# Optimization experiments

Hardware: AMD Instinct MI355X
Metric: run time of the kernel (lower is better)

## Reference

```python
import jax, jax.numpy as jnp
import numpy as np

PATCH = 768
POS = 64
HID = 512
B, N = 8, 2048


def setup_inputs() -> dict:
    key = jax.random.key(0)
    ks = jax.random.split(key, 8)
    d_in = PATCH + POS
    s = 1.0 / np.sqrt(d_in)
    return {
        "patches": jax.random.normal(ks[0], (B, N, PATCH), jnp.float32),
        "positions": jax.random.normal(ks[1], (B, N, POS), jnp.float32),
        "Wq": jax.random.uniform(ks[2], (d_in, HID), jnp.float32, -s, s),
        "bq": jax.random.uniform(ks[3], (HID,), jnp.float32, -s, s),
        "Wk": jax.random.uniform(ks[4], (d_in, HID), jnp.float32, -s, s),
        "bk": jax.random.uniform(ks[5], (d_in and HID,), jnp.float32, -s, s),
        "Wv": jax.random.uniform(ks[6], (d_in, HID), jnp.float32, -s, s),
        "bv": jax.random.uniform(ks[7], (HID,), jnp.float32, -s, s),
    }


def reference(patches, positions, Wq, bq, Wk, bk, Wv, bv):
    # concat patch features with positional features: [B, N, PATCH+POS]
    x = jnp.concatenate([patches, positions], axis=-1)
    Q = x @ Wq + bq  # [B, N, HID]
    K = x @ Wk + bk
    V = x @ Wv + bv
    scale = jnp.sqrt(jnp.asarray(HID, x.dtype))
    scores = jnp.einsum("bnd,bmd->bnm", Q, K) / scale  # [B, N, N]
    weights = jax.nn.softmax(scores, axis=-1)
    return jnp.einsum("bnm,bmd->bnd", weights, V)  # [B, N, HID]
```

## Files before the change

kernel.cpp:

```cpp
#include <hip/hip_runtime.h>
#include <hip/hip_bf16.h>
#include <math.h>

typedef __hip_bfloat16 bf16;
typedef __attribute__((ext_vector_type(4))) float f32x4;
typedef __attribute__((ext_vector_type(8))) short s16x8;

typedef const __attribute__((address_space(1))) void gvoid_t;
typedef __attribute__((address_space(3))) void lvoid_t;

__device__ __forceinline__ void gload16(const void* g, void* l) {
  __builtin_amdgcn_global_load_lds((gvoid_t*)g, (lvoid_t*)l, 16, 0, 0);
}
__device__ __forceinline__ unsigned short f2b(float f) {
  bf16 h = __float2bfloat16(f);
  return *(unsigned short*)&h;
}

__global__ __launch_bounds__(256) void prep_x(const float* __restrict__ patches,
                                              const float* __restrict__ positions,
                                              bf16* __restrict__ xb) {
  const int c = threadIdx.x;
  const bool lo = (c < 192);
  const bool hi = (c >= 192) && (c < 208);
  if (!(lo || hi)) return;
  const int dst = lo ? (c * 4) : (768 + (c - 192) * 4);
  #pragma unroll
  for (int rr = 0; rr < 8; ++rr) {
    const long long row = (long long)blockIdx.x * 8 + rr;
    const float* src = lo ? (patches + row * 768 + c * 4)
                          : (positions + row * 64 + (c - 192) * 4);
    float4 v = *(const float4*)src;
    uint2 w;
    w.x = (unsigned int)f2b(v.x) | ((unsigned int)f2b(v.y) << 16);
    w.y = (unsigned int)f2b(v.z) | ((unsigned int)f2b(v.w) << 16);
    *(uint2*)(xb + row * 832 + dst) = w;
  }
}

__global__ __launch_bounds__(256) void prep_w(const float* __restrict__ Wq,
                                              const float* __restrict__ Wk,
                                              const float* __restrict__ Wv,
                                              bf16* __restrict__ Wt) {
  __shared__ float tile[32][33];
  const int z = blockIdx.z;
  const float* W = (z == 0) ? Wq : (z == 1) ? Wk : Wv;
  bf16* T = Wt + (long long)z * 512 * 832;
  const int n0 = blockIdx.x * 32;
  const int k0 = blockIdx.y * 32;
  const int tx = threadIdx.x, ty = threadIdx.y;
  #pragma unroll
  for (int i = 0; i < 32; i += 8)
    tile[ty + i][tx] = W[(long long)(k0 + ty + i) * 512 + n0 + tx];
  __syncthreads();
  #pragma unroll
  for (int i = 0; i < 32; i += 8)
    T[(long long)(n0 + ty + i) * 832 + k0 + tx] = __float2bfloat16(tile[tx][ty + i]);
}

#define VMW5  asm volatile("s_waitcnt vmcnt(5)" ::: "memory")
#define VMW8  asm volatile("s_waitcnt vmcnt(8)" ::: "memory")
#define VMW10 asm volatile("s_waitcnt vmcnt(10)" ::: "memory")
#define PBAR do { __builtin_amdgcn_s_barrier(); __builtin_amdgcn_sched_barrier(0); } while (0)

__device__ __forceinline__ void stage_half(const bf16* src, char* lds, int stride) {
  gload16(src, lds);
  gload16(src + 64 * stride, lds + 8192);
}
__device__ __forceinline__ void stage_b192(const bf16* src, char* lds) {
  gload16(src, lds);
  gload16(src + 64 * 832, lds + 8192);
  gload16(src + 128 * 832, lds + 16384);
}
__device__ __forceinline__ void lda4(const bf16* base, int rowbase, int llo,
                                     int xk0, int xk1, s16x8 af[4][2]) {
  #pragma unroll
  for (int mf = 0; mf < 4; mf++) {
    const bf16* p = base + (rowbase + mf * 16 + llo) * 64;
    af[mf][0] = *(const s16x8*)(p + xk0);
    af[mf][1] = *(const s16x8*)(p + xk1);
  }
}
__device__ __forceinline__ void ldb2(const bf16* base, int rowbase, int llo,
                                     int xk0, int xk1, s16x8 bfr[2][2]) {
  #pragma unroll
  for (int nf = 0; nf < 2; nf++) {
    const bf16* p = base + (rowbase + nf * 16 + llo) * 64;
    bfr[nf][0] = *(const s16x8*)(p + xk0);
    bfr[nf][1] = *(const s16x8*)(p + xk1);
  }
}
__device__ __forceinline__ void ldb3(const bf16* base, int rowbase, int llo,
                                     int xk0, int xk1, s16x8 bfr[3][2]) {
  #pragma unroll
  for (int nf = 0; nf < 3; nf++) {
    const bf16* p = base + (rowbase + nf * 16 + llo) * 64;
    bfr[nf][0] = *(const s16x8*)(p + xk0);
    bfr[nf][1] = *(const s16x8*)(p + xk1);
  }
}
__device__ __forceinline__ void mma16(f32x4 acc[4][2], s16x8 af[4][2],
                                      s16x8 bfr[2][2]) {
  __builtin_amdgcn_s_setprio(1);
  #pragma unroll
  for (int mf = 0; mf < 4; mf++)
    #pragma unroll
    for (int nf = 0; nf < 2; nf++) {
      acc[mf][nf] = __builtin_amdgcn_mfma_f32_16x16x32_bf16(
          af[mf][0], bfr[nf][0], acc[mf][nf], 0, 0, 0);
      acc[mf][nf] = __builtin_amdgcn_mfma_f32_16x16x32_bf16(
          af[mf][1], bfr[nf][1], acc[mf][nf], 0, 0, 0);
    }
  __builtin_amdgcn_s_setprio(0);
}
__device__ __forceinline__ void mma24(f32x4 acc[4][3], s16x8 af[4][2],
                                      s16x8 bfr[3][2]) {
  __builtin_amdgcn_s_setprio(1);
  #pragma unroll
  for (int mf = 0; mf < 4; mf++)
    #pragma unroll
    for (int nf = 0; nf < 3; nf++) {
      acc[mf][nf] = __builtin_amdgcn_mfma_f32_16x16x32_bf16(
          af[mf][0], bfr[nf][0], acc[mf][nf], 0, 0, 0);
      acc[mf][nf] = __builtin_amdgcn_mfma_f32_16x16x32_bf16(
          af[mf][1], bfr[nf][1], acc[mf][nf], 0, 0, 0);
    }
  __builtin_amdgcn_s_setprio(0);
}

#define QKV_TILE(abuf, bbuf, bstage, ka1, kb2)                               \
  do {                                                                       \
                                                               \
    lda4(As2[abuf], wm * 64, llo, xk0, xk1, af);                             \
    ldb3(Bs3[bbuf], wn * 48, llo, xk0, xk1, bfr);                            \
    stage_half(sA + (ka1), (char*)As2[(abuf) ^ 1] + wofs, 832);              \
    stage_b192(sB + (kb2), (char*)Bs3[bstage] + wofs);                       \
    VMW5; PBAR;                                                              \
    mma24(acc[0], af, bfr);                                                  \
                               \
    lda4(As2[abuf], 128 + wm * 64, llo, xk0, xk1, af);                       \
    stage_half(sA + 128 * 832 + (ka1), (char*)As2[(abuf) ^ 1] + 16384 + wofs,\
               832);                                                         \
    VMW5; PBAR;                                                              \
    mma24(acc[1], af, bfr);                                                  \
  } while (0)

__global__ __launch_bounds__(512, 2) void gemm_qkv(
    const bf16* __restrict__ xb, const bf16* __restrict__ Wt,
    const float* __restrict__ bq, const float* __restrict__ bk,
    const float* __restrict__ bv,
    bf16* __restrict__ qk, bf16* __restrict__ vt) {
  __shared__ bf16 As2[2][256 * 64];
  __shared__ bf16 Bs3[3][192 * 64];
  const int tid = threadIdx.x;
  const int wave = tid >> 6, lane = tid & 63;
  const int llo = lane & 15, lhi = lane >> 4;
  const int wm = wave >> 2, wn = wave & 3;

  const unsigned int lin = blockIdx.x;
  const unsigned int xcd = lin & 7u, idx = lin >> 3;
  const unsigned int g = xcd * 64u + idx;
  const int bm_t = (int)(g >> 3);
  const int bn_t = (int)(g & 7u);
  const int row0 = bm_t * 256;
  const int col0 = bn_t * 192;

  const int sr = tid >> 3;
  const int kkofs = ((tid & 7) ^ (sr & 7)) << 3;
  const bf16* sA = xb + (long long)(row0 + sr) * 832 + kkofs;
  const bf16* sB = Wt + (long long)(col0 + sr) * 832 + kkofs;
  const int wofs = wave * 1024;

  const int xk0 = ((lhi ^ (llo & 7)) << 3);
  const int xk1 = (((4 + lhi) ^ (llo & 7)) << 3);

  f32x4 acc[2][4][3] = {};
  s16x8 af[4][2], bfr[3][2];

  stage_half(sA, (char*)As2[0] + wofs, 832);
  stage_b192(sB, (char*)Bs3[0] + wofs);
  stage_half(sA + 128 * 832, (char*)As2[0] + 16384 + wofs, 832);
  stage_b192(sB + 64, (char*)Bs3[1] + wofs);
  VMW5; PBAR;

  for (int jj = 0; jj < 2; ++jj) {
    const int u0 = jj * 6;
    QKV_TILE(0, 0, 2, (u0 + 1) * 64, (u0 + 2) * 64);
    QKV_TILE(1, 1, 0, (u0 + 2) * 64, (u0 + 3) * 64);
    QKV_TILE(0, 2, 1, (u0 + 3) * 64, (u0 + 4) * 64);
    QKV_TILE(1, 0, 2, (u0 + 4) * 64, (u0 + 5) * 64);
    QKV_TILE(0, 1, 0, (u0 + 5) * 64, (u0 + 6) * 64);
    QKV_TILE(1, 2, 1, (u0 + 6) * 64, ((u0 + 7) <= 12 ? (u0 + 7) * 64 : 768));
  }
  QKV_TILE(0, 0, 2, 768, 768);

  asm volatile("s_waitcnt vmcnt(0)" ::: "memory");

  #pragma unroll
  for (int qr = 0; qr < 2; qr++)
    #pragma unroll
    for (int mf = 0; mf < 4; mf++)
      #pragma unroll
      for (int nf = 0; nf < 3; nf++) {
        const int c = col0 + wn * 48 + nf * 16 + llo;
        const int z = c >> 9, cc = c & 511;
        const int grow0 = row0 + qr * 128 + wm * 64 + mf * 16 + lhi * 4;
        if (z < 2) {
          const float bb = (z ? bk : bq)[cc];
          bf16* outp = qk + (long long)z * 16384 * 512;
          #pragma unroll
          for (int r = 0; r < 4; r++)
            outp[(long long)(grow0 + r) * 512 + cc] =
                __float2bfloat16(acc[qr][mf][nf][r] + bb);
        } else {
          const int b = grow0 >> 11, j = grow0 & 2047;
          const float bb = bv[cc];
          uint2 w;
          w.x = (unsigned int)f2b(acc[qr][mf][nf][0] + bb) |
                ((unsigned int)f2b(acc[qr][mf][nf][1] + bb) << 16);
          w.y = (unsigned int)f2b(acc[qr][mf][nf][2] + bb) |
                ((unsigned int)f2b(acc[qr][mf][nf][3] + bb) << 16);
          *(uint2*)(vt + (long long)b * 512 * 2048 + (long long)cc * 2048 + j) = w;
        }
      }
}
#undef QKV_TILE

__global__ __launch_bounds__(512, 2) void gemm_scores(const bf16* __restrict__ qk,
                                                      bf16* __restrict__ S,
                                                      float* __restrict__ rowsumP) {
  __shared__ bf16 As[2][256 * 64];
  __shared__ bf16 Bs[2][256 * 64];
  const int tid = threadIdx.x;
  const int wave = tid >> 6, lane = tid & 63;
  const int llo = lane & 15, lhi = lane >> 4;
  const int wm = wave >> 2, wn = wave & 3;

  const unsigned int lin = blockIdx.x;
  const int b = (int)(lin & 7u);
  const unsigned int idx = lin >> 3;
  const int row0 = (int)(idx >> 3) * 256;
  const int coltile = (int)(idx & 7u);
  const int col0 = coltile * 256;

  const bf16* Ab = qk + (long long)b * 2048 * 512;
  const bf16* Bb = qk + (long long)16384 * 512 + (long long)b * 2048 * 512;

  const int sr = tid >> 3;
  const int kkofs = ((tid & 7) ^ (sr & 7)) << 3;
  const bf16* sA = Ab + (long long)(row0 + sr) * 512 + kkofs;
  const bf16* sB = Bb + (long long)(col0 + sr) * 512 + kkofs;
  const int wofs = wave * 1024;

  const int xk0 = ((lhi ^ (llo & 7)) << 3);
  const int xk1 = (((4 + lhi) ^ (llo & 7)) << 3);

  f32x4 acc[2][2][4][2] = {};
  s16x8 af[4][2], bf0[2][2], bf1[2][2];

  stage_half(sA, (char*)As[0] + wofs, 512);
  stage_half(sB, (char*)Bs[0] + wofs, 512);
  stage_half(sB + 128 * 512, (char*)Bs[0] + 16384 + wofs, 512);
  stage_half(sA + 128 * 512, (char*)As[0] + 16384 + wofs, 512);
  stage_half(sA + 64, (char*)As[1] + wofs, 512);
  stage_half(sB + 64, (char*)Bs[1] + wofs, 512);
  VMW8; PBAR;

  for (int i = 0; i < 4; ++i) {
    const int kt1 = (2 * i + 1) * 64;
    const int kt2 = (2 * i + 2 < 8) ? (2 * i + 2) * 64 : 448;
    const int kt3 = (2 * i + 3 < 8) ? (2 * i + 3) * 64 : 448;
    lda4(As[0], wm * 64, llo, xk0, xk1, af);
    ldb2(Bs[0], wn * 32, llo, xk0, xk1, bf0);
    stage_half(sB + 128 * 512 + kt1, (char*)Bs[1] + 16384 + wofs, 512);
    VMW8; PBAR;
    mma16(acc[0][0], af, bf0);
    ldb2(Bs[0], 128 + wn * 32, llo, xk0, xk1, bf1);
    stage_half(sA + 128 * 512 + kt1, (char*)As[1] + 16384 + wofs, 512);
    VMW8; PBAR;
    mma16(acc[0][1], af, bf1);
    lda4(As[0], 128 + wm * 64, llo, xk0, xk1, af);
    stage_half(sA + kt2, (char*)As[0] + wofs, 512);
    PBAR;
    mma16(acc[1][0], af, bf0);
    stage_half(sB + kt2, (char*)Bs[0] + wofs, 512);
    VMW8; PBAR;
    mma16(acc[1][1], af, bf1);
    lda4(As[1], wm * 64, llo, xk0, xk1, af);
    ldb2(Bs[1], wn * 32, llo, xk0, xk1, bf0);
    stage_half(sB + 128 * 512 + kt2, (char*)Bs[0] + 16384 + wofs, 512);
    VMW8; PBAR;
    mma16(acc[0][0], af, bf0);
    ldb2(Bs[1], 128 + wn * 32, llo, xk0, xk1, bf1);
    stage_half(sA + 128 * 512 + kt2, (char*)As[0] + 16384 + wofs, 512);
    VMW8; PBAR;
    mma16(acc[0][1], af, bf1);
    lda4(As[1], 128 + wm * 64, llo, xk0, xk1, af);
    stage_half(sA + kt3, (char*)As[1] + wofs, 512);
    PBAR;
    mma16(acc[1][0], af, bf0);
    stage_half(sB + kt3, (char*)Bs[1] + wofs, 512);
    VMW8; PBAR;
    mma16(acc[1][1], af, bf1);
  }

  __syncthreads();

  const float alpha = 0.044194173824159216f;
  bf16* Sb = S + (long long)b * 2048 * 2048;
  #pragma unroll
  for (int qr = 0; qr < 2; qr++)
    #pragma unroll
    for (int qc = 0; qc < 2; qc++)
      #pragma unroll
      for (int mf = 0; mf < 4; mf++)
        #pragma unroll
        for (int nf = 0; nf < 2; nf++) {
          #pragma unroll
          for (int r = 0; r < 4; r++)
            acc[qr][qc][mf][nf][r] = __expf(acc[qr][qc][mf][nf][r] * alpha);
          const int gcol = col0 + qc * 128 + wn * 32 + nf * 16 + llo;
          const int grow0 = row0 + qr * 128 + wm * 64 + mf * 16 + lhi * 4;
          #pragma unroll
          for (int r = 0; r < 4; r++)
            Sb[(long long)(grow0 + r) * 2048 + gcol] =
                __float2bfloat16(acc[qr][qc][mf][nf][r]);
        }

  float* psum = (float*)As;
  #pragma unroll
  for (int qr = 0; qr < 2; qr++)
    #pragma unroll
    for (int mf = 0; mf < 4; mf++)
      #pragma unroll
      for (int r = 0; r < 4; r++) {
        float p = acc[qr][0][mf][0][r] + acc[qr][0][mf][1][r] +
                  acc[qr][1][mf][0][r] + acc[qr][1][mf][1][r];
        p += __shfl_xor(p, 1, 64);
        p += __shfl_xor(p, 2, 64);
        p += __shfl_xor(p, 4, 64);
        p += __shfl_xor(p, 8, 64);
        if (llo == 0)
          psum[wn * 256 + qr * 128 + wm * 64 + mf * 16 + lhi * 4 + r] = p;
      }
  __syncthreads();
  if (tid < 256) {
    const float v = psum[tid] + psum[256 + tid] + psum[512 + tid] + psum[768 + tid];
    rowsumP[(long long)(b * 8 + coltile) * 2048 + row0 + tid] = v;
  }
}

__global__ __launch_bounds__(256) void reduce_rowsum(
    const float* __restrict__ rowsumP, float* __restrict__ rinv) {
  const int i = blockIdx.x * 256 + threadIdx.x;
  const int b = i >> 11, row = i & 2047;
  const float* p = rowsumP + ((long long)b * 8) * 2048 + row;
  float s = 0.f;
  #pragma unroll
  for (int t = 0; t < 8; t++) s += p[t * 2048];
  rinv[i] = 1.0f / s;
}

#define PV_TILE(c, cs, kstage)                                              \
  do {                                                                      \
                                                              \
    lda4(As3[c], wm * 64, llo, xk0, xk1, af);                               \
    ldb2(Bs3[c], wn * 32, llo, xk0, xk1, bfr);                              \
    stage_half(sA + (kstage), (char*)As3[cs] + wofs, 2048);                 \
    stage_half(sB + (kstage), (char*)Bs3[cs] + wofs, 2048);                 \
    VMW10; PBAR;                                                            \
    mma16(acc[0], af, bfr);                                                 \
                              \
    lda4(As3[c], 128 + wm * 64, llo, xk0, xk1, af);                         \
    stage_half(sA + 128 * 2048 + (kstage), (char*)As3[cs] + 16384 + wofs,   \
               2048);                                                       \
    VMW8; PBAR;                                                             \
    mma16(acc[1], af, bfr);                                                 \
  } while (0)

__global__ __launch_bounds__(512, 2) void gemm_pv(const bf16* __restrict__ S,
                                                  const bf16* __restrict__ vt,
                                                  const float* __restrict__ rinv,
                                                  float* __restrict__ out) {
  __shared__ bf16 As3[3][256 * 64];
  __shared__ bf16 Bs3[3][128 * 64];
  const int tid = threadIdx.x;
  const int wave = tid >> 6, lane = tid & 63;
  const int llo = lane & 15, lhi = lane >> 4;
  const int wm = wave >> 2, wn = wave & 3;

  const unsigned int lin = blockIdx.x;
  const int b = (int)(lin & 7u);
  const unsigned int idx = lin >> 3;
  const int row0 = (int)(idx >> 2) * 256;
  const int col0 = (int)(idx & 3u) * 128;

  const bf16* Ab = S + (long long)b * 2048 * 2048;
  const bf16* Bb = vt + (long long)b * 512 * 2048;

  const int sr = tid >> 3;
  const int kkofs = ((tid & 7) ^ (sr & 7)) << 3;
  const bf16* sA = Ab + (long long)(row0 + sr) * 2048 + kkofs;
  const bf16* sB = Bb + (long long)(col0 + sr) * 2048 + kkofs;
  const int wofs = wave * 1024;

  const int xk0 = ((lhi ^ (llo & 7)) << 3);
  const int xk1 = (((4 + lhi) ^ (llo & 7)) << 3);

  f32x4 acc[2][4][2] = {};
  s16x8 af[4][2], bfr[2][2];

  stage_half(sA, (char*)As3[0] + wofs, 2048);
  stage_half(sB, (char*)Bs3[0] + wofs, 2048);
  stage_half(sA + 128 * 2048, (char*)As3[0] + 16384 + wofs, 2048);
  stage_half(sA + 64, (char*)As3[1] + wofs, 2048);
  stage_half(sB + 64, (char*)Bs3[1] + wofs, 2048);
  stage_half(sA + 128 * 2048 + 64, (char*)As3[1] + 16384 + wofs, 2048);
  VMW8; PBAR;

  for (int j = 0; j < 10; ++j) {
    const int kb = j * 192;
    PV_TILE(0, 2, kb + 128);
    PV_TILE(1, 0, kb + 192);
    PV_TILE(2, 1, kb + 256);
  }
  PV_TILE(0, 2, 1984);
  PV_TILE(1, 0, 1984);

  asm volatile("s_waitcnt vmcnt(0)" ::: "memory");

  const float* rs = rinv + (long long)b * 2048;
  float* Ob = out + (long long)b * 2048 * 512;
  #pragma unroll
  for (int qr = 0; qr < 2; qr++)
    #pragma unroll
    for (int mf = 0; mf < 4; mf++) {
      const int grow0 = row0 + qr * 128 + wm * 64 + mf * 16 + lhi * 4;
      float iv[4];
      #pragma unroll
      for (int r = 0; r < 4; r++) iv[r] = rs[grow0 + r];
      #pragma unroll
      for (int nf = 0; nf < 2; nf++) {
        const int gcol = col0 + wn * 32 + nf * 16 + llo;
        #pragma unroll
        for (int r = 0; r < 4; r++)
          Ob[(long long)(grow0 + r) * 512 + gcol] = acc[qr][mf][nf][r] * iv[r];
      }
    }
}
#undef PV_TILE

extern "C" void kernel_launch(void* const* d_in, const int* in_sizes, int n_in,
                              void* d_out, int out_size, void* d_ws, size_t ws_size,
                              hipStream_t stream) {
  const float* patches = (const float*)d_in[0];
  const float* positions = (const float*)d_in[1];
  const float* Wq = (const float*)d_in[2];
  const float* bq = (const float*)d_in[3];
  const float* Wk = (const float*)d_in[4];
  const float* bk = (const float*)d_in[5];
  const float* Wv = (const float*)d_in[6];
  const float* bv = (const float*)d_in[7];
  float* out = (float*)d_out;

  if (ws_size < 149422080u) return;

  char* ws = (char*)d_ws;
  bf16* Wt = (bf16*)(ws);
  bf16* xb = (bf16*)(ws + 2555904);
  bf16* qk = (bf16*)(ws + 29818880);
  bf16* vt = (bf16*)(ws + 63373312);
  bf16* S  = (bf16*)(ws + 80150528);
  float* rinv    = (float*)(ws + 147259392);
  float* rowsumP = (float*)(ws + 147324928);

  prep_x<<<2048, 256, 0, stream>>>(patches, positions, xb);
  prep_w<<<dim3(16, 26, 3), dim3(32, 8), 0, stream>>>(Wq, Wk, Wv, Wt);
  gemm_qkv<<<512, 512, 0, stream>>>(xb, Wt, bq, bk, bv, qk, vt);
  gemm_scores<<<512, 512, 0, stream>>>(qk, S, rowsumP);
  reduce_rowsum<<<64, 256, 0, stream>>>(rowsumP, rinv);
  gemm_pv<<<256, 512, 0, stream>>>(S, vt, rinv, out);
}
```

Measured before the change: 262.1 us.

## Retile QKV GEMM to 256x128 with triple buffering and fuse rowsum reduction into PV

The QKV projection GEMM moves from 256x192 tiles with A double-buffered to 256x128 tiles with both A and B triple-buffered, and launches 768 blocks instead of 512. Each tile now maps to a single Q/K/V matrix, so the epilogue branch is taken once per block instead of per fragment. The separate reduce_rowsum kernel is removed; gemm_pv sums the partial row sums itself after its main loop and stores the reciprocals in LDS, saving one launch at the cost of a little redundant work per block. Smaller tiles reuse A less per block, traded for more blocks and a deeper pipeline.

```diff
diff --git a/kernel.cpp b/kernel.cpp
--- a/kernel.cpp
+++ b/kernel.cpp
@@ -58,7 +58,6 @@
     T[(long long)(n0 + ty + i) * 832 + k0 + tx] = __float2bfloat16(tile[tx][ty + i]);
 }
 
-#define VMW5  asm volatile("s_waitcnt vmcnt(5)" ::: "memory")
 #define VMW8  asm volatile("s_waitcnt vmcnt(8)" ::: "memory")
 #define VMW10 asm volatile("s_waitcnt vmcnt(10)" ::: "memory")
 #define PBAR do { __builtin_amdgcn_s_barrier(); __builtin_amdgcn_sched_barrier(0); } while (0)
@@ -66,11 +65,6 @@
 __device__ __forceinline__ void stage_half(const bf16* src, char* lds, int stride) {
   gload16(src, lds);
   gload16(src + 64 * stride, lds + 8192);
-}
-__device__ __forceinline__ void stage_b192(const bf16* src, char* lds) {
-  gload16(src, lds);
-  gload16(src + 64 * 832, lds + 8192);
-  gload16(src + 128 * 832, lds + 16384);
 }
 __device__ __forceinline__ void lda4(const bf16* base, int rowbase, int llo,
                                      int xk0, int xk1, s16x8 af[4][2]) {
@@ -85,15 +79,6 @@
                                      int xk0, int xk1, s16x8 bfr[2][2]) {
   #pragma unroll
   for (int nf = 0; nf < 2; nf++) {
-    const bf16* p = base + (rowbase + nf * 16 + llo) * 64;
-    bfr[nf][0] = *(const s16x8*)(p + xk0);
-    bfr[nf][1] = *(const s16x8*)(p + xk1);
-  }
-}
-__device__ __forceinline__ void ldb3(const bf16* base, int rowbase, int llo,
-                                     int xk0, int xk1, s16x8 bfr[3][2]) {
-  #pragma unroll
-  for (int nf = 0; nf < 3; nf++) {
     const bf16* p = base + (rowbase + nf * 16 + llo) * 64;
     bfr[nf][0] = *(const s16x8*)(p + xk0);
     bfr[nf][1] = *(const s16x8*)(p + xk1);
@@ -113,36 +98,22 @@
     }
   __builtin_amdgcn_s_setprio(0);
 }
-__device__ __forceinline__ void mma24(f32x4 acc[4][3], s16x8 af[4][2],
-                                      s16x8 bfr[3][2]) {
-  __builtin_amdgcn_s_setprio(1);
-  #pragma unroll
-  for (int mf = 0; mf < 4; mf++)
-    #pragma unroll
-    for (int nf = 0; nf < 3; nf++) {
-      acc[mf][nf] = __builtin_amdgcn_mfma_f32_16x16x32_bf16(
-          af[mf][0], bfr[nf][0], acc[mf][nf], 0, 0, 0);
-      acc[mf][nf] = __builtin_amdgcn_mfma_f32_16x16x32_bf16(
-          af[mf][1], bfr[nf][1], acc[mf][nf], 0, 0, 0);
-    }
-  __builtin_amdgcn_s_setprio(0);
-}
-
-#define QKV_TILE(abuf, bbuf, bstage, ka1, kb2)                               \
-  do {                                                                       \
-                                                               \
-    lda4(As2[abuf], wm * 64, llo, xk0, xk1, af);                             \
-    ldb3(Bs3[bbuf], wn * 48, llo, xk0, xk1, bfr);                            \
-    stage_half(sA + (ka1), (char*)As2[(abuf) ^ 1] + wofs, 832);              \
-    stage_b192(sB + (kb2), (char*)Bs3[bstage] + wofs);                       \
-    VMW5; PBAR;                                                              \
-    mma24(acc[0], af, bfr);                                                  \
-                               \
-    lda4(As2[abuf], 128 + wm * 64, llo, xk0, xk1, af);                       \
-    stage_half(sA + 128 * 832 + (ka1), (char*)As2[(abuf) ^ 1] + 16384 + wofs,\
-               832);                                                         \
-    VMW5; PBAR;                                                              \
-    mma24(acc[1], af, bfr);                                                  \
+
+#define QKV_TILE(c, cs, kstage)                                             \
+  do {                                                                      \
+                                                              \
+    lda4(As3[c], wm * 64, llo, xk0, xk1, af);                               \
+    ldb2(Bs3[c], wn * 32, llo, xk0, xk1, bfr);                              \
+    stage_half(sA + (kstage), (char*)As3[cs] + wofs, 832);                  \
+    stage_half(sB + (kstage), (char*)Bs3[cs] + wofs, 832);                  \
+    VMW10; PBAR;                                                            \
+    mma16(acc[0], af, bfr);                                                 \
+                              \
+    lda4(As3[c], 128 + wm * 64, llo, xk0, xk1, af);                         \
+    stage_half(sA + 128 * 832 + (kstage), (char*)As3[cs] + 16384 + wofs,    \
+               832);                                                        \
+    VMW8; PBAR;                                                             \
+    mma16(acc[1], af, bfr);                                                 \
   } while (0)
 
 __global__ __launch_bounds__(512, 2) void gemm_qkv(
@@ -150,8 +121,8 @@
     const float* __restrict__ bq, const float* __restrict__ bk,
     const float* __restrict__ bv,
     bf16* __restrict__ qk, bf16* __restrict__ vt) {
-  __shared__ bf16 As2[2][256 * 64];
-  __shared__ bf16 Bs3[3][192 * 64];
+  __shared__ bf16 As3[3][256 * 64];
+  __shared__ bf16 Bs3[3][128 * 64];
   const int tid = threadIdx.x;
   const int wave = tid >> 6, lane = tid & 63;
   const int llo = lane & 15, lhi = lane >> 4;
@@ -159,11 +130,13 @@
 
   const unsigned int lin = blockIdx.x;
   const unsigned int xcd = lin & 7u, idx = lin >> 3;
-  const unsigned int g = xcd * 64u + idx;
-  const int bm_t = (int)(g >> 3);
-  const int bn_t = (int)(g & 7u);
+  const unsigned int g = xcd * 96u + idx;
+  const int bm_t = (int)(g / 12u);
+  const int bn_t = (int)(g - (unsigned)bm_t * 12u);
   const int row0 = bm_t * 256;
-  const int col0 = bn_t * 192;
+  const int col0 = bn_t * 128;
+  const int z = col0 >> 9;
+  const int cc0 = col0 & 511;
 
   const int sr = tid >> 3;
   const int kkofs = ((tid & 7) ^ (sr & 7)) << 3;
@@ -174,55 +147,66 @@
   const int xk0 = ((lhi ^ (llo & 7)) << 3);
   const int xk1 = (((4 + lhi) ^ (llo & 7)) << 3);
 
-  f32x4 acc[2][4][3] = {};
-  s16x8 af[4][2], bfr[3][2];
-
-  stage_half(sA, (char*)As2[0] + wofs, 832);
-  stage_b192(sB, (char*)Bs3[0] + wofs);
-  stage_half(sA + 128 * 832, (char*)As2[0] + 16384 + wofs, 832);
-  stage_b192(sB + 64, (char*)Bs3[1] + wofs);
-  VMW5; PBAR;
-
-  for (int jj = 0; jj < 2; ++jj) {
-    const int u0 = jj * 6;
-    QKV_TILE(0, 0, 2, (u0 + 1) * 64, (u0 + 2) * 64);
-    QKV_TILE(1, 1, 0, (u0 + 2) * 64, (u0 + 3) * 64);
-    QKV_TILE(0, 2, 1, (u0 + 3) * 64, (u0 + 4) * 64);
-    QKV_TILE(1, 0, 2, (u0 + 4) * 64, (u0 + 5) * 64);
-    QKV_TILE(0, 1, 0, (u0 + 5) * 64, (u0 + 6) * 64);
-    QKV_TILE(1, 2, 1, (u0 + 6) * 64, ((u0 + 7) <= 12 ? (u0 + 7) * 64 : 768));
-  }
-  QKV_TILE(0, 0, 2, 768, 768);
+  f32x4 acc[2][4][2] = {};
+  s16x8 af[4][2], bfr[2][2];
+
+  stage_half(sA, (char*)As3[0] + wofs, 832);
+  stage_half(sB, (char*)Bs3[0] + wofs, 832);
+  stage_half(sA + 128 * 832, (char*)As3[0] + 16384 + wofs, 832);
+  stage_half(sA + 64, (char*)As3[1] + wofs, 832);
+  stage_half(sB + 64, (char*)Bs3[1] + wofs, 832);
+  stage_half(sA + 128 * 832 + 64, (char*)As3[1] + 16384 + wofs, 832);
+  VMW8; PBAR;
+
+  for (int j = 0; j < 4; ++j) {
+    const int k2 = (j * 3 + 2) * 64;
+    const int k3 = (j * 3 + 3) * 64;
+    const int k4u = (j * 3 + 4) * 64;
+    const int k4 = (k4u <= 768) ? k4u : 768;
+    QKV_TILE(0, 2, k2);
+    QKV_TILE(1, 0, k3);
+    QKV_TILE(2, 1, k4);
+  }
+  QKV_TILE(0, 2, 768);
 
   asm volatile("s_waitcnt vmcnt(0)" ::: "memory");
 
-  #pragma unroll
-  for (int qr = 0; qr < 2; qr++)
-    #pragma unroll
-    for (int mf = 0; mf < 4; mf++)
-      #pragma unroll
-      for (int nf = 0; nf < 3; nf++) {
-        const int c = col0 + wn * 48 + nf * 16 + llo;
-        const int z = c >> 9, cc = c & 511;
-        const int grow0 = row0 + qr * 128 + wm * 64 + mf * 16 + lhi * 4;
-        if (z < 2) {
-          const float bb = (z ? bk : bq)[cc];
-          bf16* outp = qk + (long long)z * 16384 * 512;
+  if (z < 2) {
+    const float* bias = z ? bk : bq;
+    bf16* outp = qk + (long long)z * 16384 * 512;
+    #pragma unroll
+    for (int qr = 0; qr < 2; qr++)
+      #pragma unroll
+      for (int mf = 0; mf < 4; mf++)
+        #pragma unroll
+        for (int nf = 0; nf < 2; nf++) {
+          const int c = cc0 + wn * 32 + nf * 16 + llo;
+          const int grow0 = row0 + qr * 128 + wm * 64 + mf * 16 + lhi * 4;
+          const float bb = bias[c];
           #pragma unroll
           for (int r = 0; r < 4; r++)
-            outp[(long long)(grow0 + r) * 512 + cc] =
+            outp[(long long)(grow0 + r) * 512 + c] =
                 __float2bfloat16(acc[qr][mf][nf][r] + bb);
-        } else {
-          const int b = grow0 >> 11, j = grow0 & 2047;
-          const float bb = bv[cc];
+        }
+  } else {
+    #pragma unroll
+    for (int qr = 0; qr < 2; qr++)
+      #pragma unroll
+      for (int mf = 0; mf < 4; mf++)
+        #pragma unroll
+        for (int nf = 0; nf < 2; nf++) {
+          const int c = cc0 + wn * 32 + nf * 16 + llo;
+          const int grow0 = row0 + qr * 128 + wm * 64 + mf * 16 + lhi * 4;
+          const int b = grow0 >> 11, jj = grow0 & 2047;
+          const float bb = bv[c];
           uint2 w;
           w.x = (unsigned int)f2b(acc[qr][mf][nf][0] + bb) |
                 ((unsigned int)f2b(acc[qr][mf][nf][1] + bb) << 16);
           w.y = (unsigned int)f2b(acc[qr][mf][nf][2] + bb) |
                 ((unsigned int)f2b(acc[qr][mf][nf][3] + bb) << 16);
-          *(uint2*)(vt + (long long)b * 512 * 2048 + (long long)cc * 2048 + j) = w;
+          *(uint2*)(vt + (long long)b * 512 * 2048 + (long long)c * 2048 + jj) = w;
         }
-      }
+  }
 }
 #undef QKV_TILE
 
@@ -348,17 +332,6 @@
     const float v = psum[tid] + psum[256 + tid] + psum[512 + tid] + psum[768 + tid];
     rowsumP[(long long)(b * 8 + coltile) * 2048 + row0 + tid] = v;
   }
-}
-
-__global__ __launch_bounds__(256) void reduce_rowsum(
-    const float* __restrict__ rowsumP, float* __restrict__ rinv) {
-  const int i = blockIdx.x * 256 + threadIdx.x;
-  const int b = i >> 11, row = i & 2047;
-  const float* p = rowsumP + ((long long)b * 8) * 2048 + row;
-  float s = 0.f;
-  #pragma unroll
-  for (int t = 0; t < 8; t++) s += p[t * 2048];
-  rinv[i] = 1.0f / s;
 }
 
 #define PV_TILE(c, cs, kstage)                                              \
@@ -380,7 +353,7 @@
 
 __global__ __launch_bounds__(512, 2) void gemm_pv(const bf16* __restrict__ S,
                                                   const bf16* __restrict__ vt,
-                                                  const float* __restrict__ rinv,
+                                                  const float* __restrict__ rowsumP,
                                                   float* __restrict__ out) {
   __shared__ bf16 As3[3][256 * 64];
   __shared__ bf16 Bs3[3][128 * 64];
@@ -428,8 +401,18 @@
   PV_TILE(1, 0, 1984);
 
   asm volatile("s_waitcnt vmcnt(0)" ::: "memory");
-
-  const float* rs = rinv + (long long)b * 2048;
+  __syncthreads();
+
+  float* rrow = (float*)As3[1];
+  if (tid < 256) {
+    const float* rp = rowsumP + ((long long)b * 8) * 2048 + row0 + tid;
+    float s = 0.f;
+    #pragma unroll
+    for (int t = 0; t < 8; t++) s += rp[t * 2048];
+    rrow[tid] = 1.0f / s;
+  }
+  __syncthreads();
+
   float* Ob = out + (long long)b * 2048 * 512;
   #pragma unroll
   for (int qr = 0; qr < 2; qr++)
@@ -438,7 +421,7 @@
       const int grow0 = row0 + qr * 128 + wm * 64 + mf * 16 + lhi * 4;
       float iv[4];
       #pragma unroll
-      for (int r = 0; r < 4; r++) iv[r] = rs[grow0 + r];
+      for (int r = 0; r < 4; r++) iv[r] = rrow[grow0 - row0 + r];
       #pragma unroll
       for (int nf = 0; nf < 2; nf++) {
         const int gcol = col0 + wn * 32 + nf * 16 + llo;
@@ -471,13 +454,11 @@
   bf16* qk = (bf16*)(ws + 29818880);
   bf16* vt = (bf16*)(ws + 63373312);
   bf16* S  = (bf16*)(ws + 80150528);
-  float* rinv    = (float*)(ws + 147259392);
   float* rowsumP = (float*)(ws + 147324928);
 
   prep_x<<<2048, 256, 0, stream>>>(patches, positions, xb);
   prep_w<<<dim3(16, 26, 3), dim3(32, 8), 0, stream>>>(Wq, Wk, Wv, Wt);
-  gemm_qkv<<<512, 512, 0, stream>>>(xb, Wt, bq, bk, bv, qk, vt);
+  gemm_qkv<<<768, 512, 0, stream>>>(xb, Wt, bq, bk, bv, qk, vt);
   gemm_scores<<<512, 512, 0, stream>>>(qk, S, rowsumP);
-  reduce_rowsum<<<64, 256, 0, stream>>>(rowsumP, rinv);
-  gemm_pv<<<256, 512, 0, stream>>>(S, vt, rinv, out);
-}
+  gemm_pv<<<256, 512, 0, stream>>>(S, vt, rowsumP, out);
+}
```

New measurement: 271.5 us. 3.6% more time.
